# Performance work log

Hardware: AMD Instinct MI355X
Metric: run time of the kernel (lower is better)

## Reference

```python
import jax, jax.numpy as jnp
import numpy as np
from jax import lax

B = 8        # number of point clouds (batch size)
N = 2048     # points per cloud (equal-size clouds)
K = 64       # max_num_neighbors in radius query
BN_EPS = 1e-5

_gather = jax.vmap(lambda a, i: a[i])  # per-batch gather: a [M,...], i [K_sel]


def _fps(p, k):
    """Farthest point sampling on p [n,3] -> [k] int32 indices (deterministic start at 0)."""
    n = p.shape[0]
    def step(carry, _):
        dist, last = carry
        d = jnp.sum((p - p[last]) ** 2, axis=-1)
        dist = jnp.minimum(dist, d)
        nxt = jnp.argmax(dist).astype(jnp.int32)
        return (dist, nxt), nxt
    init = (jnp.full((n,), 1e10, p.dtype), jnp.array(0, jnp.int32))
    _, rest = lax.scan(step, init, None, length=k - 1)
    return jnp.concatenate([jnp.zeros((1,), jnp.int32), rest])


def _ball_conv(pos, x, r, w1, b1, g, beta, m, v, w2, b2):
    """radius ball-query (self included, K nearest within r) + PointNetConv with max aggr.
    pos [B,M,3], x [B,M,C] -> [B,M,Cout]"""
    d2 = jnp.sum((pos[:, :, None, :] - pos[:, None, :, :]) ** 2, axis=-1)  # [B,M,M]
    score = jnp.where(d2 <= r * r, -d2, -jnp.inf)
    neg_d, nbr = lax.top_k(score, K)                 # [B,M,K] neighbor (source j) ids
    valid = neg_d > -jnp.inf
    x_j = _gather(x, nbr)                            # [B,M,K,C]
    pos_j = _gather(pos, nbr)                        # [B,M,K,3]
    feat = jnp.concatenate([x_j, pos_j - pos[:, :, None, :]], axis=-1)
    h = feat @ w1 + b1
    h = (h - m) / jnp.sqrt(v + BN_EPS) * g + beta    # BatchNorm1d (inference stats)
    h = jax.nn.relu(h)
    h = jax.nn.relu(h @ w2 + b2)
    h = jnp.where(valid[..., None], h, -jnp.inf)
    return jnp.max(h, axis=2)                        # max aggregation over neighbors


def setup_inputs() -> dict:
    key = jax.random.key(0)
    ks = jax.random.split(key, 20)
    def lin_w(k, fi, fo):
        return (jax.random.normal(k, (fi, fo), jnp.float32) / np.sqrt(fi)).astype(jnp.float32)
    def vec(k, d, scale=0.1):
        return (jax.random.normal(k, (d,), jnp.float32) * scale).astype(jnp.float32)
    inp = {
        'pos': jax.random.normal(ks[0], (B * N, 3), jnp.float32),
        'c1_w1': lin_w(ks[1], 6, 128),   'c1_b1': vec(ks[2], 128),
        'c1_g': jnp.ones((128,), jnp.float32) + vec(ks[3], 128),
        'c1_beta': vec(ks[4], 128),
        'c1_m': vec(ks[5], 128),
        'c1_v': jax.random.uniform(ks[6], (128,), jnp.float32, 0.5, 1.5),
        'c1_w2': lin_w(ks[7], 128, 128), 'c1_b2': vec(ks[8], 128),
        'c2_w1': lin_w(ks[9], 131, 256), 'c2_b1': vec(ks[10], 256),
        'c2_g': jnp.ones((256,), jnp.float32) + vec(ks[11], 256),
        'c2_beta': vec(ks[12], 256),
        'c2_m': vec(ks[13], 256),
        'c2_v': jax.random.uniform(ks[14], (256,), jnp.float32, 0.5, 1.5),
        'c2_w2': lin_w(ks[15], 256, 512), 'c2_b2': vec(ks[16], 512),
        'batch': jnp.repeat(jnp.arange(B, dtype=jnp.int32), N),
    }
    return inp


def reference(pos, c1_w1, c1_b1, c1_g, c1_beta, c1_m, c1_v, c1_w2, c1_b2,
              c2_w1, c2_b1, c2_g, c2_beta, c2_m, c2_v, c2_w2, c2_b2, batch):
    p = pos.reshape(B, N, 3)
    # normalize_pos: per-cloud mean / unbiased std (scatter_mean / scatter_std)
    mean = p.mean(axis=1, keepdims=True)
    var = jnp.sum((p - mean) ** 2, axis=1, keepdims=True) / (N - 1)
    p = (p - mean) / (jnp.sqrt(var) + 1e-6)
    # level 1: fps ratio=0.5, radius r=0.1
    idx1 = jax.vmap(lambda q: _fps(q, N // 2))(p)        # [B, N/2]
    pos1 = _gather(p, idx1)
    x1 = _ball_conv(pos1, pos1, 0.1, c1_w1, c1_b1, c1_g, c1_beta, c1_m, c1_v, c1_w2, c1_b2)
    # level 2: fps ratio=0.5, radius r=0.25
    idx2 = jax.vmap(lambda q: _fps(q, N // 4))(pos1)     # [B, N/4]
    pos2 = _gather(pos1, idx2)
    x2_in = _gather(x1, idx2)
    x2 = _ball_conv(pos2, x2_in, 0.25, c2_w1, c2_b1, c2_g, c2_beta, c2_m, c2_v, c2_w2, c2_b2)
    batch2 = jnp.repeat(jnp.arange(B, dtype=batch.dtype), N // 4)
    return x2.reshape(B * (N // 4), 512), batch2
```

## Files before the change

### kernel.cpp

```cpp
#include <hip/hip_runtime.h>

#define B_ 8
#define N_ 2048

#define REP8(M) M(0) M(1) M(2) M(3) M(4) M(5) M(6) M(7)

template <int CTRL>
__device__ __forceinline__ float dppMaxStep(float v) {
  int o = __builtin_amdgcn_update_dpp(__float_as_int(-1.0f), __float_as_int(v),
                                      CTRL, 0xF, 0xF, false);
  return fmaxf(v, __int_as_float(o));
}

__device__ __forceinline__ float waveMax(float v) {
  v = dppMaxStep<0x111>(v);
  v = dppMaxStep<0x112>(v);
  v = dppMaxStep<0x114>(v);
  v = dppMaxStep<0x118>(v);
  v = dppMaxStep<0x142>(v);
  v = dppMaxStep<0x143>(v);
  return v;
}

__global__ __launch_bounds__(256) void norm_fps1_kernel(const float* __restrict__ pos,
                                                        float* __restrict__ pos1) {
  __shared__ float4 Sp[2048];
  __shared__ float2 red[2][4];
  __shared__ double wsum[3][4];
  __shared__ float bc[6];
  const int b = blockIdx.x, tid = threadIdx.x;
  const float* base = pos + (size_t)b * N_ * 3;
  float px[8], py[8], pz[8];
  double sx = 0.0, sy = 0.0, sz = 0.0;
#pragma unroll
  for (int k = 0; k < 8; ++k) {
    int g = tid * 8 + k;
    px[k] = base[g * 3 + 0];
    py[k] = base[g * 3 + 1];
    pz[k] = base[g * 3 + 2];
    sx += (double)px[k]; sy += (double)py[k]; sz += (double)pz[k];
  }
  const int wid = tid >> 6, lid = tid & 63;
#pragma unroll
  for (int off = 32; off >= 1; off >>= 1) {
    sx += __shfl_down(sx, off);
    sy += __shfl_down(sy, off);
    sz += __shfl_down(sz, off);
  }
  if (lid == 0) { wsum[0][wid] = sx; wsum[1][wid] = sy; wsum[2][wid] = sz; }
  __syncthreads();
  if (tid == 0) {
    bc[0] = (float)((wsum[0][0] + wsum[0][1] + wsum[0][2] + wsum[0][3]) / 2048.0);
    bc[1] = (float)((wsum[1][0] + wsum[1][1] + wsum[1][2] + wsum[1][3]) / 2048.0);
    bc[2] = (float)((wsum[2][0] + wsum[2][1] + wsum[2][2] + wsum[2][3]) / 2048.0);
  }
  __syncthreads();
  const float mx = bc[0], my = bc[1], mz = bc[2];
  float dx[8], dy[8], dz[8];
  double qxs = 0.0, qys = 0.0, qzs = 0.0;
#pragma unroll
  for (int k = 0; k < 8; ++k) {
    dx[k] = __fsub_rn(px[k], mx);
    dy[k] = __fsub_rn(py[k], my);
    dz[k] = __fsub_rn(pz[k], mz);
    qxs += (double)__fmul_rn(dx[k], dx[k]);
    qys += (double)__fmul_rn(dy[k], dy[k]);
    qzs += (double)__fmul_rn(dz[k], dz[k]);
  }
#pragma unroll
  for (int off = 32; off >= 1; off >>= 1) {
    qxs += __shfl_down(qxs, off);
    qys += __shfl_down(qys, off);
    qzs += __shfl_down(qzs, off);
  }
  if (lid == 0) { wsum[0][wid] = qxs; wsum[1][wid] = qys; wsum[2][wid] = qzs; }
  __syncthreads();
  if (tid == 0) {
    bc[3] = __fadd_rn(__fsqrt_rn((float)((wsum[0][0]+wsum[0][1]+wsum[0][2]+wsum[0][3]) / 2047.0)), 1e-6f);
    bc[4] = __fadd_rn(__fsqrt_rn((float)((wsum[1][0]+wsum[1][1]+wsum[1][2]+wsum[1][3]) / 2047.0)), 1e-6f);
    bc[5] = __fadd_rn(__fsqrt_rn((float)((wsum[2][0]+wsum[2][1]+wsum[2][2]+wsum[2][3]) / 2047.0)), 1e-6f);
  }
  __syncthreads();
  const float isx = bc[3], isy = bc[4], isz = bc[5];
#define DECL8(i) float X##i, Y##i, Z##i, D##i;
  REP8(DECL8)
#define INIT8(i)                                                             \
  {                                                                          \
    X##i = __fdiv_rn(dx[i], isx);                                            \
    Y##i = __fdiv_rn(dy[i], isy);                                            \
    Z##i = __fdiv_rn(dz[i], isz);                                            \
    D##i = 1e10f;                                                            \
    Sp[tid * 8 + i] = make_float4(X##i, Y##i, Z##i, 0.0f);                   \
  }
  REP8(INIT8)
  __syncthreads();
  float4 q0 = Sp[0];
  float qx = q0.x, qy = q0.y, qz = q0.z;
  float* p1b = pos1 + (size_t)b * 1024 * 3;
  if (tid == 0) { p1b[0] = qx; p1b[1] = qy; p1b[2] = qz; }
  const int gbase = tid * 8;
  for (int t = 1; t < 1024; ++t) {
#define UPD8(i)                                                              \
    {                                                                        \
      float ddx = __fsub_rn(X##i, qx);                                       \
      float ddy = __fsub_rn(Y##i, qy);                                       \
      float ddz = __fsub_rn(Z##i, qz);                                       \
      float d = __fadd_rn(__fadd_rn(__fmul_rn(ddx, ddx), __fmul_rn(ddy, ddy)),\
                          __fmul_rn(ddz, ddz));                              \
      D##i = fminf(D##i, d);                                                 \
    }
    REP8(UPD8)
    float v01 = (D1 > D0) ? D1 : D0;  int g01 = (D1 > D0) ? gbase + 1 : gbase + 0;
    float v23 = (D3 > D2) ? D3 : D2;  int g23 = (D3 > D2) ? gbase + 3 : gbase + 2;
    float v45 = (D5 > D4) ? D5 : D4;  int g45 = (D5 > D4) ? gbase + 5 : gbase + 4;
    float v67 = (D7 > D6) ? D7 : D6;  int g67 = (D7 > D6) ? gbase + 7 : gbase + 6;
    float v03 = (v23 > v01) ? v23 : v01;  int g03 = (v23 > v01) ? g23 : g01;
    float v47 = (v67 > v45) ? v67 : v45;  int g47 = (v67 > v45) ? g67 : g45;
    float bv  = (v47 > v03) ? v47 : v03;  int bg  = (v47 > v03) ? g47 : g03;
    float mv = waveMax(bv);
    float vmax = __int_as_float(__builtin_amdgcn_readlane(__float_as_int(mv), 63));
    unsigned long long msk = __ballot(bv == vmax);
    int owner = __builtin_ctzll(msk);
    int gw = __builtin_amdgcn_readlane(bg, owner);
    const int par = t & 1;
    if (lid == 0) red[par][wid] = make_float2(vmax, __int_as_float(gw));
    __syncthreads();
    float2 r0 = red[par][0], r1 = red[par][1], r2 = red[par][2], r3 = red[par][3];
    float fv = r0.x; int fg = __float_as_int(r0.y);
    if (r1.x > fv) { fv = r1.x; fg = __float_as_int(r1.y); }
    if (r2.x > fv) { fv = r2.x; fg = __float_as_int(r2.y); }
    if (r3.x > fv) { fv = r3.x; fg = __float_as_int(r3.y); }
    float4 pw = Sp[fg];
    qx = pw.x; qy = pw.y; qz = pw.z;
    if (tid == 0) {
      float* pp = p1b + t * 3;
      pp[0] = qx; pp[1] = qy; pp[2] = qz;
    }
  }
}

__global__ __launch_bounds__(128) void mid_kernel(
    const float* __restrict__ pos1,
    const float* __restrict__ w1, const float* __restrict__ b1,
    const float* __restrict__ g, const float* __restrict__ beta,
    const float* __restrict__ m, const float* __restrict__ v,
    const float* __restrict__ w2, const float* __restrict__ b2,
    float* __restrict__ x1out,
    int* __restrict__ idx2, float* __restrict__ pos2) {
  __shared__ union MidU {
    struct { int nbr[64]; int cnt; float hbuf[128]; } c;
    struct { float4 Sp2[1024]; float2 red2[2][2]; } f;
  } u;
  if (blockIdx.x >= 8) {
    const int bb = blockIdx.x - 8;
    const int b = bb >> 10;
    const int i = bb & 1023;
    const int c = threadIdx.x;
    const float* pb = pos1 + (size_t)b * 1024 * 3;
    const float xi = pb[i * 3 + 0], yi = pb[i * 3 + 1], zi = pb[i * 3 + 2];
    if (c == 0) u.c.cnt = 0;
    __syncthreads();
    const float rr = (float)(0.1 * 0.1);
#pragma unroll
    for (int k = 0; k < 8; ++k) {
      int j = c + (k << 7);
      float ddx = __fsub_rn(xi, pb[j * 3 + 0]);
      float ddy = __fsub_rn(yi, pb[j * 3 + 1]);
      float ddz = __fsub_rn(zi, pb[j * 3 + 2]);
      float d2 = __fadd_rn(__fadd_rn(__fmul_rn(ddx, ddx), __fmul_rn(ddy, ddy)),
                           __fmul_rn(ddz, ddz));
      if (d2 <= rr) {
        int s = atomicAdd(&u.c.cnt, 1);
        if (s < 64) u.c.nbr[s] = j;
      }
    }
    __syncthreads();
    const int n = min(u.c.cnt, 64);
    const float scale = g[c] / sqrtf(v[c] + 1e-5f);
    const float shift = beta[c] - m[c] * scale;
    float w1c[6];
#pragma unroll
    for (int f = 0; f < 6; ++f) w1c[f] = w1[f * 128 + c];
    const float b1c = b1[c], b2c = b2[c];
    float acc = 0.0f;
    for (int qq = 0; qq < n; ++qq) {
      const int j = u.c.nbr[qq];
      const float fx = pb[j * 3 + 0], fy = pb[j * 3 + 1], fz = pb[j * 3 + 2];
      float h = b1c;
      h = fmaf(fx, w1c[0], h);
      h = fmaf(fy, w1c[1], h);
      h = fmaf(fz, w1c[2], h);
      h = fmaf(fx - xi, w1c[3], h);
      h = fmaf(fy - yi, w1c[4], h);
      h = fmaf(fz - zi, w1c[5], h);
      h = fmaxf(fmaf(h, scale, shift), 0.0f);
      u.c.hbuf[c] = h;
      __syncthreads();
      float o = b2c;
#pragma unroll 8
      for (int k2 = 0; k2 < 128; ++k2) o = fmaf(u.c.hbuf[k2], w2[(k2 << 7) + c], o);
      acc = fmaxf(acc, fmaxf(o, 0.0f));
      __syncthreads();
    }
    x1out[((size_t)(b * 1024 + i)) * 128 + c] = acc;
  } else {
    const int b = blockIdx.x;
    const int tid = threadIdx.x;
    const int wid = tid >> 6, lid = tid & 63;
    const float* p1b = pos1 + (size_t)b * 1024 * 3;
#define DECLF(i) float X##i, Y##i, Z##i, D##i;
    REP8(DECLF)
#define LOADF(i)                                                             \
    {                                                                        \
      const float* pp = p1b + (tid * 8 + i) * 3;                             \
      X##i = pp[0]; Y##i = pp[1]; Z##i = pp[2];                              \
      D##i = 1e10f;                                                          \
      u.f.Sp2[tid * 8 + i] = make_float4(X##i, Y##i, Z##i, 0.0f);            \
    }
    REP8(LOADF)
    __syncthreads();
    float4 q0 = u.f.Sp2[0];
    float qx = q0.x, qy = q0.y, qz = q0.z;
    float* p2b = pos2 + (size_t)b * 512 * 3;
    int* i2b = idx2 + b * 512;
    if (tid == 0) {
      p2b[0] = qx; p2b[1] = qy; p2b[2] = qz;
      i2b[0] = 0;
    }
    const int gbase = tid * 8;
    for (int t = 1; t < 512; ++t) {
      REP8(UPD8)
      float v01 = (D1 > D0) ? D1 : D0;  int g01 = (D1 > D0) ? gbase + 1 : gbase + 0;
      float v23 = (D3 > D2) ? D3 : D2;  int g23 = (D3 > D2) ? gbase + 3 : gbase + 2;
      float v45 = (D5 > D4) ? D5 : D4;  int g45 = (D5 > D4) ? gbase + 5 : gbase + 4;
      float v67 = (D7 > D6) ? D7 : D6;  int g67 = (D7 > D6) ? gbase + 7 : gbase + 6;
      float v03 = (v23 > v01) ? v23 : v01;  int g03 = (v23 > v01) ? g23 : g01;
      float v47 = (v67 > v45) ? v67 : v45;  int g47 = (v67 > v45) ? g67 : g45;
      float bv  = (v47 > v03) ? v47 : v03;  int bg  = (v47 > v03) ? g47 : g03;
      float mv = waveMax(bv);
      float vmax = __int_as_float(__builtin_amdgcn_readlane(__float_as_int(mv), 63));
      unsigned long long msk = __ballot(bv == vmax);
      int owner = __builtin_ctzll(msk);
      int gw = __builtin_amdgcn_readlane(bg, owner);
      const int par = t & 1;
      if (lid == 0) u.f.red2[par][wid] = make_float2(vmax, __int_as_float(gw));
      __syncthreads();
      float2 r0 = u.f.red2[par][0], r1 = u.f.red2[par][1];
      float fv = r0.x; int fg = __float_as_int(r0.y);
      if (r1.x > fv) { fv = r1.x; fg = __float_as_int(r1.y); }
      float4 pw = u.f.Sp2[fg];
      qx = pw.x; qy = pw.y; qz = pw.z;
      if (tid == 0) {
        float* pp = p2b + t * 3;
        pp[0] = qx; pp[1] = qy; pp[2] = qz;
        i2b[t] = fg;
      }
    }
  }
}

__global__ __launch_bounds__(256) void conv2_kernel(
    const float* __restrict__ pos2, const int* __restrict__ idx2,
    const float* __restrict__ x1,
    const float* __restrict__ w1, const float* __restrict__ b1,
    const float* __restrict__ g, const float* __restrict__ beta,
    const float* __restrict__ m, const float* __restrict__ v,
    const float* __restrict__ w2, const float* __restrict__ b2,
    float* __restrict__ out, float* __restrict__ bout) {
  const int b = blockIdx.x >> 9;
  const int i = blockIdx.x & 511;
  const int c = threadIdx.x;
  __shared__ int nbr[64];
  __shared__ int cnt;
  __shared__ float xj[128];
  __shared__ float hbuf[256];
  const float* pb = pos2 + (size_t)b * 512 * 3;
  const float xi = pb[i * 3 + 0], yi = pb[i * 3 + 1], zi = pb[i * 3 + 2];
  if (c == 0) cnt = 0;
  __syncthreads();
  const float rr = (float)(0.25 * 0.25);
#pragma unroll
  for (int k = 0; k < 2; ++k) {
    int j = c + (k << 8);
    float ddx = __fsub_rn(xi, pb[j * 3 + 0]);
    float ddy = __fsub_rn(yi, pb[j * 3 + 1]);
    float ddz = __fsub_rn(zi, pb[j * 3 + 2]);
    float d2 = __fadd_rn(__fadd_rn(__fmul_rn(ddx, ddx), __fmul_rn(ddy, ddy)),
                         __fmul_rn(ddz, ddz));
    if (d2 <= rr) {
      int s = atomicAdd(&cnt, 1);
      if (s < 64) nbr[s] = j;
    }
  }
  __syncthreads();
  const int n = min(cnt, 64);
  const float scale = g[c] / sqrtf(v[c] + 1e-5f);
  const float shift = beta[c] - m[c] * scale;
  const float b1c = b1[c];
  const float b2c0 = b2[c], b2c1 = b2[c + 256];
  float acc0 = 0.0f, acc1 = 0.0f;
  for (int q = 0; q < n; ++q) {
    const int j = nbr[q];
    const int src = idx2[b * 512 + j];
    if (c < 128) xj[c] = x1[((size_t)b * 1024 + src) * 128 + c];
    const float fx = pb[j * 3 + 0], fy = pb[j * 3 + 1], fz = pb[j * 3 + 2];
    const float r0 = fx - xi, r1 = fy - yi, r2 = fz - zi;
    __syncthreads();
    float h = b1c;
#pragma unroll 8
    for (int f = 0; f < 128; ++f) h = fmaf(xj[f], w1[f * 256 + c], h);
    h = fmaf(r0, w1[128 * 256 + c], h);
    h = fmaf(r1, w1[129 * 256 + c], h);
    h = fmaf(r2, w1[130 * 256 + c], h);
    h = fmaxf(fmaf(h, scale, shift), 0.0f);
    hbuf[c] = h;
    __syncthreads();
    float o0 = b2c0, o1 = b2c1;
#pragma unroll 8
    for (int k2 = 0; k2 < 256; ++k2) {
      float hk = hbuf[k2];
      o0 = fmaf(hk, w2[k2 * 512 + c], o0);
      o1 = fmaf(hk, w2[k2 * 512 + c + 256], o1);
    }
    acc0 = fmaxf(acc0, fmaxf(o0, 0.0f));
    acc1 = fmaxf(acc1, fmaxf(o1, 0.0f));
    __syncthreads();
  }
  float* ob = out + ((size_t)(b * 512 + i)) * 512;
  ob[c] = acc0;
  ob[c + 256] = acc1;
  if (c == 0) bout[b * 512 + i] = (float)b;
}

extern "C" void kernel_launch(void* const* d_in, const int* in_sizes, int n_in,
                              void* d_out, int out_size, void* d_ws, size_t ws_size,
                              hipStream_t stream) {
  const float* pos    = (const float*)d_in[0];
  const float* c1_w1  = (const float*)d_in[1];
  const float* c1_b1  = (const float*)d_in[2];
  const float* c1_g   = (const float*)d_in[3];
  const float* c1_be  = (const float*)d_in[4];
  const float* c1_m   = (const float*)d_in[5];
  const float* c1_v   = (const float*)d_in[6];
  const float* c1_w2  = (const float*)d_in[7];
  const float* c1_b2  = (const float*)d_in[8];
  const float* c2_w1  = (const float*)d_in[9];
  const float* c2_b1  = (const float*)d_in[10];
  const float* c2_g   = (const float*)d_in[11];
  const float* c2_be  = (const float*)d_in[12];
  const float* c2_m   = (const float*)d_in[13];
  const float* c2_v   = (const float*)d_in[14];
  const float* c2_w2  = (const float*)d_in[15];
  const float* c2_b2  = (const float*)d_in[16];

  char* ws = (char*)d_ws;
  float* pos1 = (float*)(ws + 0);
  int*   idx2 = (int*)  (ws + 98304);
  float* pos2 = (float*)(ws + 114688);
  float* x1   = (float*)(ws + 163840);
  float* out  = (float*)d_out;

  norm_fps1_kernel<<<8, 256, 0, stream>>>(pos, pos1);
  mid_kernel<<<8 + 8192, 128, 0, stream>>>(pos1, c1_w1, c1_b1, c1_g, c1_be,
                                           c1_m, c1_v, c1_w2, c1_b2, x1, idx2, pos2);
  conv2_kernel<<<4096, 256, 0, stream>>>(pos2, idx2, x1, c2_w1, c2_b1, c2_g,
                                         c2_be, c2_m, c2_v, c2_w2, c2_b2, out,
                                         out + 2097152);
}
```

Measured before the change: 830.1 us.

## Batch conv2 edges across eight centers and carry coordinates through FPS reductions

The level-2 conv now gives each block eight query centers and pools all their neighbor edges, then runs both MLP layers on eight edges per pass, so every w1 and w2 weight load is reused eight times instead of once. The grid shrinks from 4096 to 512 blocks. Both FPS loops now pass the winning point's coordinates through the DPP wave reduction, with an index tie-break, which removes the ballot/readlane step and the shared-memory position table lookup. FPS results are staged in shared memory and written to global memory once at the end. Risks are fewer blocks, higher register pressure and extra padding work for centers with few neighbors.

```diff
diff --git a/kernel.cpp b/kernel.cpp
--- a/kernel.cpp
+++ b/kernel.cpp
@@ -6,28 +6,66 @@
 #define REP8(M) M(0) M(1) M(2) M(3) M(4) M(5) M(6) M(7)
 
 template <int CTRL>
-__device__ __forceinline__ float dppMaxStep(float v) {
-  int o = __builtin_amdgcn_update_dpp(__float_as_int(-1.0f), __float_as_int(v),
-                                      CTRL, 0xF, 0xF, false);
-  return fmaxf(v, __int_as_float(o));
+__device__ __forceinline__ void dpp5(float& v, int& g, float& x, float& y, float& z) {
+  int ov_ = __builtin_amdgcn_update_dpp(__float_as_int(-1.0f), __float_as_int(v),
+                                        CTRL, 0xF, 0xF, false);
+  int og_ = __builtin_amdgcn_update_dpp(0x7fffffff, g, CTRL, 0xF, 0xF, false);
+  int ox_ = __builtin_amdgcn_update_dpp(0, __float_as_int(x), CTRL, 0xF, 0xF, false);
+  int oy_ = __builtin_amdgcn_update_dpp(0, __float_as_int(y), CTRL, 0xF, 0xF, false);
+  int oz_ = __builtin_amdgcn_update_dpp(0, __float_as_int(z), CTRL, 0xF, 0xF, false);
+  float ov = __int_as_float(ov_);
+  bool p = (ov > v) || ((ov == v) && (og_ < g));
+  v = p ? ov : v;
+  g = p ? og_ : g;
+  x = p ? __int_as_float(ox_) : x;
+  y = p ? __int_as_float(oy_) : y;
+  z = p ? __int_as_float(oz_) : z;
 }
 
-__device__ __forceinline__ float waveMax(float v) {
-  v = dppMaxStep<0x111>(v);
-  v = dppMaxStep<0x112>(v);
-  v = dppMaxStep<0x114>(v);
-  v = dppMaxStep<0x118>(v);
-  v = dppMaxStep<0x142>(v);
-  v = dppMaxStep<0x143>(v);
-  return v;
-}
-
-__global__ __launch_bounds__(256) void norm_fps1_kernel(const float* __restrict__ pos,
-                                                        float* __restrict__ pos1) {
-  __shared__ float4 Sp[2048];
-  __shared__ float2 red[2][4];
+#define UPD8(i)                                                               \
+  {                                                                           \
+    float ddx = __fsub_rn(X##i, qx);                                          \
+    float ddy = __fsub_rn(Y##i, qy);                                          \
+    float ddz = __fsub_rn(Z##i, qz);                                          \
+    float d = __fadd_rn(__fadd_rn(__fmul_rn(ddx, ddx), __fmul_rn(ddy, ddy)),  \
+                        __fmul_rn(ddz, ddz));                                 \
+    D##i = fminf(D##i, d);                                                    \
+  }
+
+#define LANE_TREE8                                                            \
+  bool pA = (D1 > D0);                                                        \
+  float vA = pA ? D1 : D0; int gA = gbase + (pA ? 1 : 0);                     \
+  float xA = pA ? X1 : X0, yA = pA ? Y1 : Y0, zA = pA ? Z1 : Z0;              \
+  bool pB = (D3 > D2);                                                        \
+  float vB = pB ? D3 : D2; int gB = gbase + (pB ? 3 : 2);                     \
+  float xB = pB ? X3 : X2, yB = pB ? Y3 : Y2, zB = pB ? Z3 : Z2;              \
+  bool pC = (D5 > D4);                                                        \
+  float vC = pC ? D5 : D4; int gC = gbase + (pC ? 5 : 4);                     \
+  float xC = pC ? X5 : X4, yC = pC ? Y5 : Y4, zC = pC ? Z5 : Z4;              \
+  bool pD = (D7 > D6);                                                        \
+  float vD = pD ? D7 : D6; int gD = gbase + (pD ? 7 : 6);                     \
+  float xD = pD ? X7 : X6, yD = pD ? Y7 : Y6, zD = pD ? Z7 : Z6;              \
+  bool pE = (vB > vA);                                                        \
+  float vE = pE ? vB : vA; int gE = pE ? gB : gA;                             \
+  float xE = pE ? xB : xA, yE = pE ? yB : yA, zE = pE ? zB : zA;              \
+  bool pF = (vD > vC);                                                        \
+  float vF = pF ? vD : vC; int gF = pF ? gD : gC;                             \
+  float xF = pF ? xD : xC, yF = pF ? yD : yC, zF = pF ? zD : zC;              \
+  bool pG = (vF > vE);                                                        \
+  float bv = pG ? vF : vE; int bg = pG ? gF : gE;                            \
+  float bx = pG ? xF : xE, by = pG ? yF : yE, bz = pG ? zF : zE;
+
+#define DPP_CHAIN  dpp5<0x111>(bv, bg, bx, by, bz); dpp5<0x112>(bv, bg, bx, by, bz); \
+                   dpp5<0x114>(bv, bg, bx, by, bz); dpp5<0x118>(bv, bg, bx, by, bz); \
+                   dpp5<0x142>(bv, bg, bx, by, bz); dpp5<0x143>(bv, bg, bx, by, bz);
+
+__global__ __launch_bounds__(256, 1) void norm_fps1_kernel(const float* __restrict__ pos,
+                                                           float* __restrict__ pos1) {
+  __shared__ float outP[1024 * 3];
+  __shared__ float4 redA[2][4];
+  __shared__ float redB[2][4];
   __shared__ double wsum[3][4];
-  __shared__ float bc[6];
+  __shared__ float bc[9];
   const int b = blockIdx.x, tid = threadIdx.x;
   const float* base = pos + (size_t)b * N_ * 3;
   float px[8], py[8], pz[8];
@@ -84,59 +122,47 @@
   const float isx = bc[3], isy = bc[4], isz = bc[5];
 #define DECL8(i) float X##i, Y##i, Z##i, D##i;
   REP8(DECL8)
-#define INIT8(i)                                                             \
-  {                                                                          \
-    X##i = __fdiv_rn(dx[i], isx);                                            \
-    Y##i = __fdiv_rn(dy[i], isy);                                            \
-    Z##i = __fdiv_rn(dz[i], isz);                                            \
-    D##i = 1e10f;                                                            \
-    Sp[tid * 8 + i] = make_float4(X##i, Y##i, Z##i, 0.0f);                   \
+#define INIT8(i)                                                              \
+  {                                                                           \
+    X##i = __fdiv_rn(dx[i], isx);                                             \
+    Y##i = __fdiv_rn(dy[i], isy);                                             \
+    Z##i = __fdiv_rn(dz[i], isz);                                             \
+    D##i = 1e10f;                                                             \
   }
   REP8(INIT8)
-  __syncthreads();
-  float4 q0 = Sp[0];
-  float qx = q0.x, qy = q0.y, qz = q0.z;
-  float* p1b = pos1 + (size_t)b * 1024 * 3;
-  if (tid == 0) { p1b[0] = qx; p1b[1] = qy; p1b[2] = qz; }
+  if (tid == 0) { bc[6] = X0; bc[7] = Y0; bc[8] = Z0; }
+  __syncthreads();
+  float qx = bc[6], qy = bc[7], qz = bc[8];
+  if (tid == 0) { outP[0] = qx; outP[1] = qy; outP[2] = qz; }
   const int gbase = tid * 8;
   for (int t = 1; t < 1024; ++t) {
-#define UPD8(i)                                                              \
-    {                                                                        \
-      float ddx = __fsub_rn(X##i, qx);                                       \
-      float ddy = __fsub_rn(Y##i, qy);                                       \
-      float ddz = __fsub_rn(Z##i, qz);                                       \
-      float d = __fadd_rn(__fadd_rn(__fmul_rn(ddx, ddx), __fmul_rn(ddy, ddy)),\
-                          __fmul_rn(ddz, ddz));                              \
-      D##i = fminf(D##i, d);                                                 \
-    }
     REP8(UPD8)
-    float v01 = (D1 > D0) ? D1 : D0;  int g01 = (D1 > D0) ? gbase + 1 : gbase + 0;
-    float v23 = (D3 > D2) ? D3 : D2;  int g23 = (D3 > D2) ? gbase + 3 : gbase + 2;
-    float v45 = (D5 > D4) ? D5 : D4;  int g45 = (D5 > D4) ? gbase + 5 : gbase + 4;
-    float v67 = (D7 > D6) ? D7 : D6;  int g67 = (D7 > D6) ? gbase + 7 : gbase + 6;
-    float v03 = (v23 > v01) ? v23 : v01;  int g03 = (v23 > v01) ? g23 : g01;
-    float v47 = (v67 > v45) ? v67 : v45;  int g47 = (v67 > v45) ? g67 : g45;
-    float bv  = (v47 > v03) ? v47 : v03;  int bg  = (v47 > v03) ? g47 : g03;
-    float mv = waveMax(bv);
-    float vmax = __int_as_float(__builtin_amdgcn_readlane(__float_as_int(mv), 63));
-    unsigned long long msk = __ballot(bv == vmax);
-    int owner = __builtin_ctzll(msk);
-    int gw = __builtin_amdgcn_readlane(bg, owner);
+    LANE_TREE8
+    DPP_CHAIN
     const int par = t & 1;
-    if (lid == 0) red[par][wid] = make_float2(vmax, __int_as_float(gw));
-    __syncthreads();
-    float2 r0 = red[par][0], r1 = red[par][1], r2 = red[par][2], r3 = red[par][3];
-    float fv = r0.x; int fg = __float_as_int(r0.y);
-    if (r1.x > fv) { fv = r1.x; fg = __float_as_int(r1.y); }
-    if (r2.x > fv) { fv = r2.x; fg = __float_as_int(r2.y); }
-    if (r3.x > fv) { fv = r3.x; fg = __float_as_int(r3.y); }
-    float4 pw = Sp[fg];
-    qx = pw.x; qy = pw.y; qz = pw.z;
-    if (tid == 0) {
-      float* pp = p1b + t * 3;
-      pp[0] = qx; pp[1] = qy; pp[2] = qz;
-    }
-  }
+    if (lid == 63) {
+      redA[par][wid] = make_float4(bv, __int_as_float(bg), bx, by);
+      redB[par][wid] = bz;
+    }
+    __syncthreads();
+    float4 s0 = redA[par][0];
+    float fv = s0.x; int fg = __float_as_int(s0.y);
+    float fx = s0.z, fy = s0.w, fz = redB[par][0];
+#pragma unroll
+    for (int w = 1; w < 4; ++w) {
+      float4 sw = redA[par][w];
+      float zw = redB[par][w];
+      int gww = __float_as_int(sw.y);
+      bool p = (sw.x > fv) || ((sw.x == fv) && (gww < fg));
+      fv = p ? sw.x : fv; fg = p ? gww : fg;
+      fx = p ? sw.z : fx; fy = p ? sw.w : fy; fz = p ? zw : fz;
+    }
+    qx = fx; qy = fy; qz = fz;
+    if (tid == 0) { outP[t * 3 + 0] = qx; outP[t * 3 + 1] = qy; outP[t * 3 + 2] = qz; }
+  }
+  __syncthreads();
+  float* p1b = pos1 + (size_t)b * 1024 * 3;
+  for (int i = tid; i < 3072; i += 256) p1b[i] = outP[i];
 }
 
 __global__ __launch_bounds__(128) void mid_kernel(
@@ -149,7 +175,7 @@
     int* __restrict__ idx2, float* __restrict__ pos2) {
   __shared__ union MidU {
     struct { int nbr[64]; int cnt; float hbuf[128]; } c;
-    struct { float4 Sp2[1024]; float2 red2[2][2]; } f;
+    struct { float outP[512 * 3]; int outI[512]; float4 redA[2][2]; float redB[2][2]; float q0[3]; } s;
   } u;
   if (blockIdx.x >= 8) {
     const int bb = blockIdx.x - 8;
@@ -208,58 +234,58 @@
     const int tid = threadIdx.x;
     const int wid = tid >> 6, lid = tid & 63;
     const float* p1b = pos1 + (size_t)b * 1024 * 3;
-#define DECLF(i) float X##i, Y##i, Z##i, D##i;
-    REP8(DECLF)
-#define LOADF(i)                                                             \
-    {                                                                        \
-      const float* pp = p1b + (tid * 8 + i) * 3;                             \
-      X##i = pp[0]; Y##i = pp[1]; Z##i = pp[2];                              \
-      D##i = 1e10f;                                                          \
-      u.f.Sp2[tid * 8 + i] = make_float4(X##i, Y##i, Z##i, 0.0f);            \
-    }
-    REP8(LOADF)
-    __syncthreads();
-    float4 q0 = u.f.Sp2[0];
-    float qx = q0.x, qy = q0.y, qz = q0.z;
-    float* p2b = pos2 + (size_t)b * 512 * 3;
-    int* i2b = idx2 + b * 512;
+    REP8(DECL8)
+#define LOADF2(i)                                                             \
+    {                                                                         \
+      const float* pp = p1b + (tid * 8 + i) * 3;                              \
+      X##i = pp[0]; Y##i = pp[1]; Z##i = pp[2];                               \
+      D##i = 1e10f;                                                           \
+    }
+    REP8(LOADF2)
+    if (tid == 0) { u.s.q0[0] = X0; u.s.q0[1] = Y0; u.s.q0[2] = Z0; }
+    __syncthreads();
+    float qx = u.s.q0[0], qy = u.s.q0[1], qz = u.s.q0[2];
     if (tid == 0) {
-      p2b[0] = qx; p2b[1] = qy; p2b[2] = qz;
-      i2b[0] = 0;
+      u.s.outP[0] = qx; u.s.outP[1] = qy; u.s.outP[2] = qz;
+      u.s.outI[0] = 0;
     }
     const int gbase = tid * 8;
     for (int t = 1; t < 512; ++t) {
       REP8(UPD8)
-      float v01 = (D1 > D0) ? D1 : D0;  int g01 = (D1 > D0) ? gbase + 1 : gbase + 0;
-      float v23 = (D3 > D2) ? D3 : D2;  int g23 = (D3 > D2) ? gbase + 3 : gbase + 2;
-      float v45 = (D5 > D4) ? D5 : D4;  int g45 = (D5 > D4) ? gbase + 5 : gbase + 4;
-      float v67 = (D7 > D6) ? D7 : D6;  int g67 = (D7 > D6) ? gbase + 7 : gbase + 6;
-      float v03 = (v23 > v01) ? v23 : v01;  int g03 = (v23 > v01) ? g23 : g01;
-      float v47 = (v67 > v45) ? v67 : v45;  int g47 = (v67 > v45) ? g67 : g45;
-      float bv  = (v47 > v03) ? v47 : v03;  int bg  = (v47 > v03) ? g47 : g03;
-      float mv = waveMax(bv);
-      float vmax = __int_as_float(__builtin_amdgcn_readlane(__float_as_int(mv), 63));
-      unsigned long long msk = __ballot(bv == vmax);
-      int owner = __builtin_ctzll(msk);
-      int gw = __builtin_amdgcn_readlane(bg, owner);
+      LANE_TREE8
+      DPP_CHAIN
       const int par = t & 1;
-      if (lid == 0) u.f.red2[par][wid] = make_float2(vmax, __int_as_float(gw));
+      if (lid == 63) {
+        u.s.redA[par][wid] = make_float4(bv, __int_as_float(bg), bx, by);
+        u.s.redB[par][wid] = bz;
+      }
       __syncthreads();
-      float2 r0 = u.f.red2[par][0], r1 = u.f.red2[par][1];
-      float fv = r0.x; int fg = __float_as_int(r0.y);
-      if (r1.x > fv) { fv = r1.x; fg = __float_as_int(r1.y); }
-      float4 pw = u.f.Sp2[fg];
-      qx = pw.x; qy = pw.y; qz = pw.z;
+      float4 s0 = u.s.redA[par][0];
+      float fv = s0.x; int fg = __float_as_int(s0.y);
+      float fx = s0.z, fy = s0.w, fz = u.s.redB[par][0];
+      {
+        float4 sw = u.s.redA[par][1];
+        float zw = u.s.redB[par][1];
+        int gww = __float_as_int(sw.y);
+        bool p = (sw.x > fv) || ((sw.x == fv) && (gww < fg));
+        fv = p ? sw.x : fv; fg = p ? gww : fg;
+        fx = p ? sw.z : fx; fy = p ? sw.w : fy; fz = p ? zw : fz;
+      }
+      qx = fx; qy = fy; qz = fz;
       if (tid == 0) {
-        float* pp = p2b + t * 3;
-        pp[0] = qx; pp[1] = qy; pp[2] = qz;
-        i2b[t] = fg;
+        u.s.outP[t * 3 + 0] = qx; u.s.outP[t * 3 + 1] = qy; u.s.outP[t * 3 + 2] = qz;
+        u.s.outI[t] = fg;
       }
     }
+    __syncthreads();
+    float* p2b = pos2 + (size_t)b * 512 * 3;
+    int* i2b = idx2 + b * 512;
+    for (int i = tid; i < 1536; i += 128) p2b[i] = u.s.outP[i];
+    for (int i = tid; i < 512; i += 128) i2b[i] = u.s.outI[i];
   }
 }
 
-__global__ __launch_bounds__(256) void conv2_kernel(
+__global__ __launch_bounds__(256, 2) void conv2_kernel(
     const float* __restrict__ pos2, const int* __restrict__ idx2,
     const float* __restrict__ x1,
     const float* __restrict__ w1, const float* __restrict__ b1,
@@ -267,69 +293,139 @@
     const float* __restrict__ m, const float* __restrict__ v,
     const float* __restrict__ w2, const float* __restrict__ b2,
     float* __restrict__ out, float* __restrict__ bout) {
-  const int b = blockIdx.x >> 9;
-  const int i = blockIdx.x & 511;
+  __shared__ float4 ppos[512];
+  __shared__ unsigned pool[512];
+  __shared__ int cnt[8];
+  __shared__ int pcnt;
+  __shared__ float4 xjT[128][2];
+  __shared__ float4 hT[256][2];
+  const int b = blockIdx.x >> 6;
+  const int grp = blockIdx.x & 63;
   const int c = threadIdx.x;
-  __shared__ int nbr[64];
-  __shared__ int cnt;
-  __shared__ float xj[128];
-  __shared__ float hbuf[256];
   const float* pb = pos2 + (size_t)b * 512 * 3;
-  const float xi = pb[i * 3 + 0], yi = pb[i * 3 + 1], zi = pb[i * 3 + 2];
-  if (c == 0) cnt = 0;
-  __syncthreads();
-  const float rr = (float)(0.25 * 0.25);
+  if (c < 8) cnt[c] = 0;
+  if (c == 0) pcnt = 0;
 #pragma unroll
   for (int k = 0; k < 2; ++k) {
     int j = c + (k << 8);
-    float ddx = __fsub_rn(xi, pb[j * 3 + 0]);
-    float ddy = __fsub_rn(yi, pb[j * 3 + 1]);
-    float ddz = __fsub_rn(zi, pb[j * 3 + 2]);
-    float d2 = __fadd_rn(__fadd_rn(__fmul_rn(ddx, ddx), __fmul_rn(ddy, ddy)),
-                         __fmul_rn(ddz, ddz));
-    if (d2 <= rr) {
-      int s = atomicAdd(&cnt, 1);
-      if (s < 64) nbr[s] = j;
-    }
-  }
-  __syncthreads();
-  const int n = min(cnt, 64);
+    ppos[j] = make_float4(pb[j * 3 + 0], pb[j * 3 + 1], pb[j * 3 + 2], 0.0f);
+  }
+  __syncthreads();
+  const float rr = (float)(0.25 * 0.25);
+#pragma unroll
+  for (int t = 0; t < 8; ++t) {
+    float4 pi = ppos[(grp << 3) + t];
+#pragma unroll
+    for (int k = 0; k < 2; ++k) {
+      int j = c + (k << 8);
+      float4 pj = ppos[j];
+      float ddx = __fsub_rn(pi.x, pj.x);
+      float ddy = __fsub_rn(pi.y, pj.y);
+      float ddz = __fsub_rn(pi.z, pj.z);
+      float d2 = __fadd_rn(__fadd_rn(__fmul_rn(ddx, ddx), __fmul_rn(ddy, ddy)),
+                           __fmul_rn(ddz, ddz));
+      if (d2 <= rr) {
+        int s = atomicAdd(&cnt[t], 1);
+        if (s < 64) {
+          int pe = atomicAdd(&pcnt, 1);
+          pool[pe] = ((unsigned)t << 16) | (unsigned)j;
+        }
+      }
+    }
+  }
+  __syncthreads();
+  const int nE = pcnt;
   const float scale = g[c] / sqrtf(v[c] + 1e-5f);
   const float shift = beta[c] - m[c] * scale;
   const float b1c = b1[c];
+  const float wr0 = w1[128 * 256 + c], wr1 = w1[129 * 256 + c], wr2 = w1[130 * 256 + c];
   const float b2c0 = b2[c], b2c1 = b2[c + 256];
-  float acc0 = 0.0f, acc1 = 0.0f;
-  for (int q = 0; q < n; ++q) {
-    const int j = nbr[q];
-    const int src = idx2[b * 512 + j];
-    if (c < 128) xj[c] = x1[((size_t)b * 1024 + src) * 128 + c];
-    const float fx = pb[j * 3 + 0], fy = pb[j * 3 + 1], fz = pb[j * 3 + 2];
-    const float r0 = fx - xi, r1 = fy - yi, r2 = fz - zi;
-    __syncthreads();
-    float h = b1c;
-#pragma unroll 8
-    for (int f = 0; f < 128; ++f) h = fmaf(xj[f], w1[f * 256 + c], h);
-    h = fmaf(r0, w1[128 * 256 + c], h);
-    h = fmaf(r1, w1[129 * 256 + c], h);
-    h = fmaf(r2, w1[130 * 256 + c], h);
-    h = fmaxf(fmaf(h, scale, shift), 0.0f);
-    hbuf[c] = h;
-    __syncthreads();
-    float o0 = b2c0, o1 = b2c1;
+#define ACCD(i) float A0##i = 0.0f, A1##i = 0.0f;
+  REP8(ACCD)
+  const int half = c >> 7, cc = c & 127;
+  for (int basee = 0; basee < nE; basee += 8) {
+    int E0, E1, E2, E3, E4, E5, E6, E7;
+#define LOADE(i) E##i = (basee + i < nE) ? (int)pool[basee + i] : -1;
+    REP8(LOADE)
+#pragma unroll
+    for (int rp = 0; rp < 4; ++rp) {
+      int r = (rp << 1) + half;
+      int er = r == 0 ? E0 : r == 1 ? E1 : r == 2 ? E2 : r == 3 ? E3
+             : r == 4 ? E4 : r == 5 ? E5 : r == 6 ? E6 : E7;
+      int j = (er >= 0) ? (er & 0xffff) : 0;
+      int src = idx2[b * 512 + j];
+      ((float*)&xjT[cc][0])[r] = x1[((size_t)b * 1024 + src) * 128 + cc];
+    }
+    __syncthreads();
+#define HDECL(i) float H##i = b1c;
+    REP8(HDECL)
+#pragma unroll 16
+    for (int f = 0; f < 128; ++f) {
+      float wf = w1[f * 256 + c];
+      float4 xa = xjT[f][0], xb = xjT[f][1];
+      H0 = fmaf(xa.x, wf, H0); H1 = fmaf(xa.y, wf, H1);
+      H2 = fmaf(xa.z, wf, H2); H3 = fmaf(xa.w, wf, H3);
+      H4 = fmaf(xb.x, wf, H4); H5 = fmaf(xb.y, wf, H5);
+      H6 = fmaf(xb.z, wf, H6); H7 = fmaf(xb.w, wf, H7);
+    }
+#define RELBN(i)                                                              \
+    {                                                                         \
+      int e = E##i;                                                           \
+      int jj = (e >= 0) ? (e & 0xffff) : 0;                                   \
+      int tt = (e >= 0) ? (e >> 16) : 0;                                      \
+      float4 pj = ppos[jj];                                                   \
+      float4 pi = ppos[(grp << 3) + tt];                                      \
+      H##i = fmaf(pj.x - pi.x, wr0, H##i);                                    \
+      H##i = fmaf(pj.y - pi.y, wr1, H##i);                                    \
+      H##i = fmaf(pj.z - pi.z, wr2, H##i);                                    \
+      H##i = fmaxf(fmaf(H##i, scale, shift), 0.0f);                           \
+    }
+    REP8(RELBN)
+    hT[c][0] = make_float4(H0, H1, H2, H3);
+    hT[c][1] = make_float4(H4, H5, H6, H7);
+    __syncthreads();
+#define ODECL(i) float O0##i = 0.0f, O1##i = 0.0f;
+    REP8(ODECL)
 #pragma unroll 8
     for (int k2 = 0; k2 < 256; ++k2) {
-      float hk = hbuf[k2];
-      o0 = fmaf(hk, w2[k2 * 512 + c], o0);
-      o1 = fmaf(hk, w2[k2 * 512 + c + 256], o1);
-    }
-    acc0 = fmaxf(acc0, fmaxf(o0, 0.0f));
-    acc1 = fmaxf(acc1, fmaxf(o1, 0.0f));
-    __syncthreads();
-  }
-  float* ob = out + ((size_t)(b * 512 + i)) * 512;
-  ob[c] = acc0;
-  ob[c + 256] = acc1;
-  if (c == 0) bout[b * 512 + i] = (float)b;
+      float w2a = w2[k2 * 512 + c];
+      float w2b = w2[k2 * 512 + c + 256];
+      float4 ha = hT[k2][0], hb = hT[k2][1];
+      O00 = fmaf(ha.x, w2a, O00); O10 = fmaf(ha.x, w2b, O10);
+      O01 = fmaf(ha.y, w2a, O01); O11 = fmaf(ha.y, w2b, O11);
+      O02 = fmaf(ha.z, w2a, O02); O12 = fmaf(ha.z, w2b, O12);
+      O03 = fmaf(ha.w, w2a, O03); O13 = fmaf(ha.w, w2b, O13);
+      O04 = fmaf(hb.x, w2a, O04); O14 = fmaf(hb.x, w2b, O14);
+      O05 = fmaf(hb.y, w2a, O05); O15 = fmaf(hb.y, w2b, O15);
+      O06 = fmaf(hb.z, w2a, O06); O16 = fmaf(hb.z, w2b, O16);
+      O07 = fmaf(hb.w, w2a, O07); O17 = fmaf(hb.w, w2b, O17);
+    }
+#define MERGEE(i)                                                             \
+    if (E##i >= 0) {                                                          \
+      int tt = E##i >> 16;                                                    \
+      float m0 = fmaxf(fmaf(O0##i, 1.0f, b2c0), 0.0f);                        \
+      float m1 = fmaxf(fmaf(O1##i, 1.0f, b2c1), 0.0f);                        \
+      if (tt == 0) { A00 = fmaxf(A00, m0); A10 = fmaxf(A10, m1); }            \
+      else if (tt == 1) { A01 = fmaxf(A01, m0); A11 = fmaxf(A11, m1); }       \
+      else if (tt == 2) { A02 = fmaxf(A02, m0); A12 = fmaxf(A12, m1); }       \
+      else if (tt == 3) { A03 = fmaxf(A03, m0); A13 = fmaxf(A13, m1); }       \
+      else if (tt == 4) { A04 = fmaxf(A04, m0); A14 = fmaxf(A14, m1); }       \
+      else if (tt == 5) { A05 = fmaxf(A05, m0); A15 = fmaxf(A15, m1); }       \
+      else { A06 = (tt == 6) ? fmaxf(A06, m0) : A06;                          \
+             A16 = (tt == 6) ? fmaxf(A16, m1) : A16;                          \
+             A07 = (tt == 7) ? fmaxf(A07, m0) : A07;                          \
+             A17 = (tt == 7) ? fmaxf(A17, m1) : A17; }                        \
+    }
+    REP8(MERGEE)
+  }
+#define WROUT(i)                                                              \
+  {                                                                           \
+    float* ob = out + ((size_t)(b * 512 + (grp << 3) + i)) * 512;             \
+    ob[c] = A0##i;                                                            \
+    ob[c + 256] = A1##i;                                                      \
+  }
+  REP8(WROUT)
+  if (c < 8) bout[b * 512 + (grp << 3) + c] = (float)b;
 }
 
 extern "C" void kernel_launch(void* const* d_in, const int* in_sizes, int n_in,
@@ -363,7 +459,7 @@
   norm_fps1_kernel<<<8, 256, 0, stream>>>(pos, pos1);
   mid_kernel<<<8 + 8192, 128, 0, stream>>>(pos1, c1_w1, c1_b1, c1_g, c1_be,
                                            c1_m, c1_v, c1_w2, c1_b2, x1, idx2, pos2);
-  conv2_kernel<<<4096, 256, 0, stream>>>(pos2, idx2, x1, c2_w1, c2_b1, c2_g,
-                                         c2_be, c2_m, c2_v, c2_w2, c2_b2, out,
-                                         out + 2097152);
+  conv2_kernel<<<512, 256, 0, stream>>>(pos2, idx2, x1, c2_w1, c2_b1, c2_g,
+                                        c2_be, c2_m, c2_v, c2_w2, c2_b2, out,
+                                        out + 2097152);
 }
```

New measurement: 1.596 ms. 1.92x slower.
